# Optimization experiments

Measured on AMD Instinct MI355X. Metric: run time of the kernel, lower is better.

The kernel has to match this reference:

```python
import jax, jax.numpy as jnp
import numpy as np

H = 16
HIDDEN = 1024
B, S = 2, 2048


def setup_inputs() -> dict:
    key = jax.random.key(0)
    ks = jax.random.split(key, 6)
    return {
        "query": jax.random.normal(ks[0], (B, S, HIDDEN), dtype=jnp.float32),
        "key": jax.random.normal(ks[1], (B, S, HIDDEN), dtype=jnp.float32),
        "value": jax.random.normal(ks[2], (B, S, HIDDEN), dtype=jnp.float32),
        "W_query": jax.random.normal(ks[3], (HIDDEN, HIDDEN), dtype=jnp.float32) * 0.01,
        "W_key": jax.random.normal(ks[4], (HIDDEN, HIDDEN), dtype=jnp.float32) * 0.01,
        "W_value": jax.random.normal(ks[5], (HIDDEN, HIDDEN), dtype=jnp.float32) * 0.01,
        "ln_gamma": jnp.ones((HIDDEN,), dtype=jnp.float32),
        "ln_beta": jnp.zeros((HIDDEN,), dtype=jnp.float32),
        "mask": 1,
    }


def reference(query, key, value, W_query, W_key, W_value, ln_gamma, ln_beta, mask):
    b, s, hidden = query.shape
    d = hidden // H  # chunk_size per head
    # project then split last dim into heads, head axis leading: [h, b, s, d]
    def heads(x, W):
        return jnp.transpose((x @ W).reshape(b, s, H, d), (2, 0, 1, 3))
    q = heads(query, W_query)
    k = heads(key, W_key)
    v = heads(value, W_value)
    scale = jnp.asarray(np.sqrt(d), dtype=query.dtype)
    scores = jnp.einsum("hbqd,hbkd->hbqk", q, k) / scale
    aw = jax.nn.softmax(scores, axis=-1)
    if mask:
        tril = jnp.tril(jnp.ones((s, s), dtype=aw.dtype))  # post-softmax mask
        aw = aw * tril
        aw = aw / jnp.sum(aw, axis=3, keepdims=True)
    ws = jnp.einsum("hbqk,hbkd->hbqd", aw, v)
    # concat heads back on last dim: [b, s, hidden]
    ws = jnp.transpose(ws, (1, 2, 0, 3)).reshape(b, s, hidden)
    out = ws + query
    # LayerNorm over last dim, eps=1e-5 (torch default)
    mean = jnp.mean(out, axis=-1, keepdims=True)
    var = jnp.mean(jnp.square(out - mean), axis=-1, keepdims=True)
    out = (out - mean) / jnp.sqrt(var + 1e-5) * ln_gamma + ln_beta
    return out, aw
```

## Files before the change

kernel.cpp:

```cpp
#include <hip/hip_runtime.h>

typedef unsigned short ushort_t;
typedef __attribute__((ext_vector_type(4))) float f32x4;
typedef __attribute__((ext_vector_type(4))) unsigned short u16x4;
typedef __attribute__((ext_vector_type(8))) short short8;
typedef __attribute__((ext_vector_type(8))) unsigned short ushort8;

#define B_DIM 2
#define S_LEN 2048
#define HID 1024
#define NH 16
#define HD 64
#define NROWS (B_DIM * S_LEN)

__device__ __forceinline__ ushort_t f2bf(float f) {
  union { float f; unsigned u; } v; v.f = f;
  unsigned r = v.u + 0x7FFFu + ((v.u >> 16) & 1u);
  return (ushort_t)(r >> 16);
}

__device__ __forceinline__ float bf2f(ushort_t h) {
  union { unsigned u; float f; } v;
  v.u = ((unsigned)h) << 16;
  return v.f;
}

__device__ __forceinline__ f32x4 zero4() {
  f32x4 z = {0.f, 0.f, 0.f, 0.f};
  return z;
}

__device__ __forceinline__ unsigned pk2(float a, float b) {
  unsigned r;
  asm("v_cvt_pk_bf16_f32 %0, %1, %2" : "=v"(r) : "v"(a), "v"(b));
  return r;
}

struct WcArgs { const float* W[3]; ushort_t* T[3]; };

__global__ __launch_bounds__(256) void wconv_kernel(WcArgs args) {
  __shared__ ushort_t L[64 * 65];
  const int k0 = blockIdx.x * 64, n0 = blockIdx.y * 64;
  const float* __restrict__ W = args.W[blockIdx.z];
  ushort_t* __restrict__ T = args.T[blockIdx.z];
  const int tid = threadIdx.x;
  for (int i = 0; i < 4; ++i) {
    int idx = i * 256 + tid;
    int row = idx >> 4;
    int f4  = idx & 15;
    f32x4 v = *(const f32x4*)(W + (size_t)(k0 + row) * HID + n0 + f4 * 4);
    for (int j = 0; j < 4; ++j)
      L[(f4 * 4 + j) * 65 + row] = f2bf(v[j]);
  }
  __syncthreads();
  for (int i = 0; i < 2; ++i) {
    int idx = i * 256 + tid;
    int row = idx >> 3;
    int seg = idx & 7;
    ushort8 u;
    for (int j = 0; j < 8; ++j) u[j] = L[row * 65 + seg * 8 + j];
    *(ushort8*)(T + (size_t)(n0 + row) * HID + k0 + seg * 8) = u;
  }
}

struct PgArgs { const float* A[3]; const ushort_t* Wt[3]; ushort_t* C[3]; };

__global__ __launch_bounds__(256) void proj_gemm(PgArgs args) {
  __shared__ ushort_t As[128 * 64];
  __shared__ ushort_t Bs[128 * 64];
  const int z = blockIdx.z;
  const float* __restrict__ A = args.A[z];
  const ushort_t* __restrict__ Wt = args.Wt[z];
  ushort_t* __restrict__ C = args.C[z];
  const int tid = threadIdx.x;
  const int w = tid >> 6, lane = tid & 63, g = lane >> 4, c = lane & 15;
  const int wm = w >> 1, wn = w & 1;
  const int m0 = blockIdx.y * 128, n0 = blockIdx.x * 128;
  const int swz = (c & 7) << 3;

  f32x4 acc[4][4];
  for (int mi = 0; mi < 4; ++mi)
    for (int ni = 0; ni < 4; ++ni) acc[mi][ni] = zero4();

  for (int kt = 0; kt < 16; ++kt) {
    const int k0 = kt * 64;
    __syncthreads();
    for (int i = 0; i < 4; ++i) {
      int idx = i * 256 + tid;
      int row = idx >> 3, seg = idx & 7;
      const float* src = A + (size_t)(m0 + row) * HID + k0 + seg * 8;
      f32x4 a0 = *(const f32x4*)src;
      f32x4 a1 = *(const f32x4*)(src + 4);
      ushort8 u;
      u[0] = f2bf(a0[0]); u[1] = f2bf(a0[1]); u[2] = f2bf(a0[2]); u[3] = f2bf(a0[3]);
      u[4] = f2bf(a1[0]); u[5] = f2bf(a1[1]); u[6] = f2bf(a1[2]); u[7] = f2bf(a1[3]);
      *(ushort8*)&As[row * 64 + ((seg * 8) ^ ((row & 7) << 3))] = u;
    }
    for (int i = 0; i < 4; ++i) {
      int idx = i * 256 + tid;
      int row = idx >> 3, seg = idx & 7;
      ushort8 u = *(const ushort8*)(Wt + (size_t)(n0 + row) * HID + k0 + seg * 8);
      *(ushort8*)&Bs[row * 64 + ((seg * 8) ^ ((row & 7) << 3))] = u;
    }
    __syncthreads();
    for (int ks = 0; ks < 2; ++ks) {
      short8 af[4], bf4[4];
      for (int mi = 0; mi < 4; ++mi)
        af[mi] = *(const short8*)&As[(wm * 64 + mi * 16 + c) * 64 + ((ks * 32 + 8 * g) ^ swz)];
      for (int ni = 0; ni < 4; ++ni)
        bf4[ni] = *(const short8*)&Bs[(wn * 64 + ni * 16 + c) * 64 + ((ks * 32 + 8 * g) ^ swz)];
      for (int mi = 0; mi < 4; ++mi)
        for (int ni = 0; ni < 4; ++ni)
          acc[mi][ni] = __builtin_amdgcn_mfma_f32_16x16x32_bf16(af[mi], bf4[ni], acc[mi][ni], 0, 0, 0);
    }
  }
  for (int mi = 0; mi < 4; ++mi)
    for (int ni = 0; ni < 4; ++ni)
      for (int r = 0; r < 4; ++r)
        C[(size_t)(m0 + wm * 64 + mi * 16 + 4 * g + r) * HID + n0 + wn * 64 + ni * 16 + c] =
            f2bf(acc[mi][ni][r]);
}

__global__ __launch_bounds__(256) void vtrans_kernel(const ushort_t* __restrict__ Vb,
                                                     ushort_t* __restrict__ VT) {
  __shared__ ushort_t L[64 * 72];
  const int s0 = blockIdx.x * 64, hb = blockIdx.y;
  const int h = hb >> 1, b = hb & 1;
  const int tid = threadIdx.x;
#pragma unroll
  for (int i = 0; i < 2; ++i) {
    int idx = i * 256 + tid;
    int sr = idx >> 3, seg = idx & 7;
    ushort8 u = *(const ushort8*)(Vb + ((size_t)(b * S_LEN) + s0 + sr) * HID + h * HD + seg * 8);
    *(ushort8*)&L[sr * 72 + seg * 8] = u;
  }
  __syncthreads();
#pragma unroll
  for (int i = 0; i < 2; ++i) {
    int idx = i * 256 + tid;
    int d = idx >> 3, seg2 = idx & 7;
    ushort8 u;
#pragma unroll
    for (int j = 0; j < 8; ++j) u[j] = L[(seg2 * 8 + j) * 72 + d];
    *(ushort8*)(VT + ((size_t)hb * HD + d) * S_LEN + s0 + seg2 * 8) = u;
  }
}

#define C2S 0.18033688011112042f

__device__ __forceinline__ void qkt_tile(const ushort_t* Ks, int g, int c,
                                         const short8 qB[2], f32x4 st[4]) {
#pragma unroll
  for (int nf = 0; nf < 4; ++nf) st[nf] = zero4();
#pragma unroll
  for (int ks = 0; ks < 2; ++ks) {
#pragma unroll
    for (int nf = 0; nf < 4; ++nf) {
      short8 kf = *(const short8*)&Ks[(nf * 16 + c) * 64 + 8 * ((4 * ks + g) ^ (c & 7))];
      st[nf] = __builtin_amdgcn_mfma_f32_16x16x32_bf16(kf, qB[ks], st[nf], 0, 0, 0);
    }
  }
}

__device__ __forceinline__ float tile_sum(const f32x4 st[4], int g, int c, int wq, bool diag) {
  float s = 0.f;
#pragma unroll
  for (int nf = 0; nf < 4; ++nf)
#pragma unroll
    for (int r = 0; r < 4; ++r) {
      float e = exp2f(st[nf][r] * C2S);
      bool m = diag && (nf * 16 + 4 * g + r > wq);
      s += m ? 0.f : e;
    }
  return s;
}

__device__ __forceinline__ void tile_p_pv(const f32x4 st[4], float linv, int g, int c,
                                          bool diag, int wq, float* __restrict__ awrow,
                                          char* psb, const short8 vf[2][4], f32x4 oacc[4]) {
#pragma unroll
  for (int nf = 0; nf < 4; ++nf) {
    f32x4 pv;
#pragma unroll
    for (int r = 0; r < 4; ++r) {
      float e = exp2f(st[nf][r] * C2S) * linv;
      bool m = diag && (nf * 16 + 4 * g + r > wq);
      pv[r] = m ? 0.f : e;
    }
    *(f32x4*)(awrow + nf * 16 + 4 * g) = pv;
    uint2 u;
    u.x = pk2(pv[0], pv[1]);
    u.y = pk2(pv[2], pv[3]);
    *(uint2*)(psb + (c * 128 + ((32 * nf + 8 * g) ^ ((c & 7) << 4)))) = u;
  }
#pragma unroll
  for (int ks = 0; ks < 2; ++ks) {
    short8 pf = *(const short8*)(psb + (c * 128 + ((64 * ks + 16 * g) ^ ((c & 7) << 4))));
#pragma unroll
    for (int nf = 0; nf < 4; ++nf)
      oacc[nf] = __builtin_amdgcn_mfma_f32_16x16x32_bf16(vf[ks][nf], pf, oacc[nf], 0, 0, 0);
  }
}

__global__ __launch_bounds__(256) void attn_kernel(const ushort_t* __restrict__ Qb,
    const ushort_t* __restrict__ Kb, const ushort_t* __restrict__ VT,
    float* __restrict__ aw, ushort_t* __restrict__ wsa) {
  __shared__ ushort_t Ks[64 * 64];
  __shared__ ushort_t Vt[64 * 64];
  __shared__ ushort_t Ps[4 * 16 * 64];

  const int tid = threadIdx.x;
  const int w = tid >> 6, lane = tid & 63, g = lane >> 4, c = lane & 15;
  const int p = blockIdx.x, hb = blockIdx.y;
  const int h = hb >> 1, b = hb & 1;
  const int lo = p, hi = 31 - p;
  const int wq = w * 16 + c;
  const int srow = tid >> 3, sseg = tid & 7;

  short8 qlo[2], qhi[2];
  {
    const ushort_t* qp = Qb + ((size_t)(b * S_LEN) + lo * 64 + wq) * HID + h * HD + 8 * g;
    qlo[0] = *(const short8*)qp;
    qlo[1] = *(const short8*)(qp + 32);
    const ushort_t* qp2 = Qb + ((size_t)(b * S_LEN) + hi * 64 + wq) * HID + h * HD + 8 * g;
    qhi[0] = *(const short8*)qp2;
    qhi[1] = *(const short8*)(qp2 + 32);
  }

  ushort8 kr[2], vr[2], kn[2], vn[2];

#pragma unroll
  for (int i = 0; i < 2; ++i) {
    int row = i * 32 + srow;
    kr[i] = *(const ushort8*)(Kb + ((size_t)(b * S_LEN) + row) * HID + h * HD + sseg * 8);
  }
#pragma unroll
  for (int i = 0; i < 2; ++i) {
    int row = i * 32 + srow;
    *(ushort8*)&Ks[row * 64 + 8 * (sseg ^ (row & 7))] = kr[i];
  }
  __syncthreads();

  float ps_lo = 0.f, ps_hi = 0.f;
  for (int kt = 0; kt <= hi; ++kt) {
    if (kt < hi) {
#pragma unroll
      for (int i = 0; i < 2; ++i) {
        int row = i * 32 + srow;
        kn[i] = *(const ushort8*)(Kb + ((size_t)(b * S_LEN) + (kt + 1) * 64 + row) * HID + h * HD + sseg * 8);
      }
    }
    f32x4 st[4];
    qkt_tile(Ks, g, c, qhi, st);
    ps_hi += tile_sum(st, g, c, wq, kt == hi);
    if (kt <= lo) {
      qkt_tile(Ks, g, c, qlo, st);
      ps_lo += tile_sum(st, g, c, wq, kt == lo);
    }
    __syncthreads();
    if (kt < hi) {
#pragma unroll
      for (int i = 0; i < 2; ++i) {
        int row = i * 32 + srow;
        *(ushort8*)&Ks[row * 64 + 8 * (sseg ^ (row & 7))] = kn[i];
      }
    }
    __syncthreads();
  }
  ps_lo += __shfl_xor(ps_lo, 16); ps_lo += __shfl_xor(ps_lo, 32);
  ps_hi += __shfl_xor(ps_hi, 16); ps_hi += __shfl_xor(ps_hi, 32);
  const float linv_lo = 1.0f / ps_lo, linv_hi = 1.0f / ps_hi;

  f32x4 oLo[4], oHi[4];
#pragma unroll
  for (int nf = 0; nf < 4; ++nf) { oLo[nf] = zero4(); oHi[nf] = zero4(); }

#pragma unroll
  for (int i = 0; i < 2; ++i) {
    int row = i * 32 + srow;
    kr[i] = *(const ushort8*)(Kb + ((size_t)(b * S_LEN) + row) * HID + h * HD + sseg * 8);
    vr[i] = *(const ushort8*)(VT + ((size_t)hb * HD + row) * S_LEN + sseg * 8);
  }
#pragma unroll
  for (int i = 0; i < 2; ++i) {
    int row = i * 32 + srow;
    *(ushort8*)&Ks[row * 64 + 8 * (sseg ^ (row & 7))] = kr[i];
    *(ushort8*)&Vt[row * 64 + 8 * (sseg ^ (row & 7))] = vr[i];
  }
  __syncthreads();

  char* psb = (char*)Ps + w * 2048;
  for (int kt = 0; kt <= hi; ++kt) {
    const int kc0 = kt * 64;
    if (kt < hi) {
#pragma unroll
      for (int i = 0; i < 2; ++i) {
        int row = i * 32 + srow;
        kn[i] = *(const ushort8*)(Kb + ((size_t)(b * S_LEN) + kc0 + 64 + row) * HID + h * HD + sseg * 8);
        vn[i] = *(const ushort8*)(VT + ((size_t)hb * HD + row) * S_LEN + kc0 + 64 + sseg * 8);
      }
    }
    short8 vf[2][4];
#pragma unroll
    for (int ks = 0; ks < 2; ++ks)
#pragma unroll
      for (int nf = 0; nf < 4; ++nf)
        vf[ks][nf] = *(const short8*)&Vt[(nf * 16 + c) * 64 + 8 * ((4 * ks + g) ^ (c & 7))];

    f32x4 st[4];
    qkt_tile(Ks, g, c, qhi, st);
    {
      float* awrow = aw + ((size_t)hb * S_LEN + hi * 64 + wq) * S_LEN + kc0;
      tile_p_pv(st, linv_hi, g, c, kt == hi, wq, awrow, psb, vf, oHi);
    }
    if (kt <= lo) {
      qkt_tile(Ks, g, c, qlo, st);
      float* awrow = aw + ((size_t)hb * S_LEN + lo * 64 + wq) * S_LEN + kc0;
      tile_p_pv(st, linv_lo, g, c, kt == lo, wq, awrow, psb, vf, oLo);
    }
    __syncthreads();
    if (kt < hi) {
#pragma unroll
      for (int i = 0; i < 2; ++i) {
        int row = i * 32 + srow;
        *(ushort8*)&Ks[row * 64 + 8 * (sseg ^ (row & 7))] = kn[i];
        *(ushort8*)&Vt[row * 64 + 8 * (sseg ^ (row & 7))] = vn[i];
      }
    }
    __syncthreads();
  }

#pragma unroll
  for (int nf = 0; nf < 4; ++nf) {
    uint2 uh, ul;
    uh.x = pk2(oHi[nf][0], oHi[nf][1]); uh.y = pk2(oHi[nf][2], oHi[nf][3]);
    ul.x = pk2(oLo[nf][0], oLo[nf][1]); ul.y = pk2(oLo[nf][2], oLo[nf][3]);
    *(uint2*)(wsa + ((size_t)(b * S_LEN) + hi * 64 + wq) * HID + h * HD + nf * 16 + 4 * g) = uh;
    *(uint2*)(wsa + ((size_t)(b * S_LEN) + lo * 64 + wq) * HID + h * HD + nf * 16 + 4 * g) = ul;
  }

  const f32x4 zz = zero4();
#pragma unroll
  for (int t = 0; t < 2; ++t) {
    const int tIdx = t ? hi : lo;
    const int z0q = (tIdx + 1) * 16;
    for (int rr = 0; rr < 16; ++rr) {
      f32x4* rowp = (f32x4*)(aw + ((size_t)hb * S_LEN + tIdx * 64 + w * 16 + rr) * S_LEN);
      for (int c4 = z0q + lane; c4 < 512; c4 += 64) rowp[c4] = zz;
    }
  }
}

__global__ __launch_bounds__(256) void ln_kernel(const ushort_t* __restrict__ wsa,
    const float* __restrict__ qin, const float* __restrict__ gamma,
    const float* __restrict__ beta, float* __restrict__ out) {
  __shared__ float red[8];
  const int row = blockIdx.x, tid = threadIdx.x;
  const size_t base = (size_t)row * HID + tid * 4;
  u16x4 xh = *(const u16x4*)(wsa + base);
  f32x4 qv = *(const f32x4*)(qin + base);
  f32x4 x;
  for (int j = 0; j < 4; ++j) x[j] = bf2f(xh[j]) + qv[j];
  float s = x[0] + x[1] + x[2] + x[3];
  float sq = x[0] * x[0] + x[1] * x[1] + x[2] * x[2] + x[3] * x[3];
  for (int m = 1; m <= 32; m <<= 1) {
    s += __shfl_xor(s, m);
    sq += __shfl_xor(sq, m);
  }
  if ((tid & 63) == 0) {
    red[(tid >> 6) * 2] = s;
    red[(tid >> 6) * 2 + 1] = sq;
  }
  __syncthreads();
  s = red[0] + red[2] + red[4] + red[6];
  sq = red[1] + red[3] + red[5] + red[7];
  const float mean = s * (1.0f / HID);
  const float var = sq * (1.0f / HID) - mean * mean;
  const float rstd = 1.0f / sqrtf(var + 1e-5f);
  f32x4 gm = *(const f32x4*)(gamma + tid * 4);
  f32x4 bt = *(const f32x4*)(beta + tid * 4);
  f32x4 o;
  for (int j = 0; j < 4; ++j) o[j] = (x[j] - mean) * rstd * gm[j] + bt[j];
  *(f32x4*)(out + base) = o;
}

extern "C" void kernel_launch(void* const* d_in, const int* in_sizes, int n_in,
                              void* d_out, int out_size, void* d_ws, size_t ws_size,
                              hipStream_t stream) {
  (void)in_sizes; (void)n_in; (void)out_size; (void)ws_size;
  const float* q_in = (const float*)d_in[0];
  const float* k_in = (const float*)d_in[1];
  const float* v_in = (const float*)d_in[2];
  const float* wq   = (const float*)d_in[3];
  const float* wk   = (const float*)d_in[4];
  const float* wv   = (const float*)d_in[5];
  const float* gamma = (const float*)d_in[6];
  const float* beta  = (const float*)d_in[7];

  ushort_t* base = (ushort_t*)d_ws;
  ushort_t* Wt0 = base;
  ushort_t* Wt1 = Wt0 + 1048576;
  ushort_t* Wt2 = Wt1 + 1048576;
  ushort_t* Qb = Wt2 + 1048576;
  ushort_t* Kb = Qb + 4194304;
  ushort_t* Vb = Kb + 4194304;
  ushort_t* VT = Vb + 4194304;
  ushort_t* wsa = VT + 4194304;

  float* out = (float*)d_out;
  float* aw = out + (size_t)NROWS * HID;

  WcArgs wc{{wq, wk, wv}, {Wt0, Wt1, Wt2}};
  wconv_kernel<<<dim3(16, 16, 3), 256, 0, stream>>>(wc);

  PgArgs pg{{q_in, k_in, v_in}, {Wt0, Wt1, Wt2}, {Qb, Kb, Vb}};
  proj_gemm<<<dim3(8, 32, 3), 256, 0, stream>>>(pg);

  vtrans_kernel<<<dim3(32, 32), 256, 0, stream>>>(Vb, VT);

  attn_kernel<<<dim3(16, 32), 256, 0, stream>>>(Qb, Kb, VT, aw, wsa);

  ln_kernel<<<dim3(NROWS), 256, 0, stream>>>(wsa, q_in, gamma, beta, out);
}
```

Baseline: 725.2 us.

## Load K/V fragments directly from global memory, drop LDS staging and barriers

```diff
diff --git a/kernel.cpp b/kernel.cpp
--- a/kernel.cpp
+++ b/kernel.cpp
@@ -148,18 +148,15 @@
 
 #define C2S 0.18033688011112042f
 
-__device__ __forceinline__ void qkt_tile(const ushort_t* Ks, int g, int c,
-                                         const short8 qB[2], f32x4 st[4]) {
+__device__ __forceinline__ void qkt_tile2(const short8 kf[2][4], const short8 qB[2],
+                                          f32x4 st[4]) {
 #pragma unroll
   for (int nf = 0; nf < 4; ++nf) st[nf] = zero4();
 #pragma unroll
-  for (int ks = 0; ks < 2; ++ks) {
-#pragma unroll
-    for (int nf = 0; nf < 4; ++nf) {
-      short8 kf = *(const short8*)&Ks[(nf * 16 + c) * 64 + 8 * ((4 * ks + g) ^ (c & 7))];
-      st[nf] = __builtin_amdgcn_mfma_f32_16x16x32_bf16(kf, qB[ks], st[nf], 0, 0, 0);
-    }
-  }
+  for (int ks = 0; ks < 2; ++ks)
+#pragma unroll
+    for (int nf = 0; nf < 4; ++nf)
+      st[nf] = __builtin_amdgcn_mfma_f32_16x16x32_bf16(kf[ks][nf], qB[ks], st[nf], 0, 0, 0);
 }
 
 __device__ __forceinline__ float tile_sum(const f32x4 st[4], int g, int c, int wq, bool diag) {
@@ -193,6 +190,7 @@
     u.y = pk2(pv[2], pv[3]);
     *(uint2*)(psb + (c * 128 + ((32 * nf + 8 * g) ^ ((c & 7) << 4)))) = u;
   }
+  __builtin_amdgcn_s_setprio(1);
 #pragma unroll
   for (int ks = 0; ks < 2; ++ks) {
     short8 pf = *(const short8*)(psb + (c * 128 + ((64 * ks + 16 * g) ^ ((c & 7) << 4))));
@@ -200,22 +198,22 @@
     for (int nf = 0; nf < 4; ++nf)
       oacc[nf] = __builtin_amdgcn_mfma_f32_16x16x32_bf16(vf[ks][nf], pf, oacc[nf], 0, 0, 0);
   }
+  __builtin_amdgcn_s_setprio(0);
 }
 
 __global__ __launch_bounds__(256) void attn_kernel(const ushort_t* __restrict__ Qb,
     const ushort_t* __restrict__ Kb, const ushort_t* __restrict__ VT,
     float* __restrict__ aw, ushort_t* __restrict__ wsa) {
-  __shared__ ushort_t Ks[64 * 64];
-  __shared__ ushort_t Vt[64 * 64];
   __shared__ ushort_t Ps[4 * 16 * 64];
 
   const int tid = threadIdx.x;
   const int w = tid >> 6, lane = tid & 63, g = lane >> 4, c = lane & 15;
-  const int p = blockIdx.x, hb = blockIdx.y;
+  const int bid = blockIdx.y * 16 + blockIdx.x;
+  const int newid = (bid & 7) * 64 + (bid >> 3);
+  const int p = newid & 15, hb = newid >> 4;
   const int h = hb >> 1, b = hb & 1;
   const int lo = p, hi = 31 - p;
   const int wq = w * 16 + c;
-  const int srow = tid >> 3, sseg = tid & 7;
 
   short8 qlo[2], qhi[2];
   {
@@ -227,45 +225,25 @@
     qhi[1] = *(const short8*)(qp2 + 32);
   }
 
-  ushort8 kr[2], vr[2], kn[2], vn[2];
-
-#pragma unroll
-  for (int i = 0; i < 2; ++i) {
-    int row = i * 32 + srow;
-    kr[i] = *(const ushort8*)(Kb + ((size_t)(b * S_LEN) + row) * HID + h * HD + sseg * 8);
-  }
-#pragma unroll
-  for (int i = 0; i < 2; ++i) {
-    int row = i * 32 + srow;
-    *(ushort8*)&Ks[row * 64 + 8 * (sseg ^ (row & 7))] = kr[i];
-  }
-  __syncthreads();
+  const ushort_t* kbase = Kb + (size_t)(b * S_LEN) * HID + h * HD;
+  const ushort_t* vtb = VT + (size_t)hb * HD * S_LEN;
 
   float ps_lo = 0.f, ps_hi = 0.f;
   for (int kt = 0; kt <= hi; ++kt) {
-    if (kt < hi) {
-#pragma unroll
-      for (int i = 0; i < 2; ++i) {
-        int row = i * 32 + srow;
-        kn[i] = *(const ushort8*)(Kb + ((size_t)(b * S_LEN) + (kt + 1) * 64 + row) * HID + h * HD + sseg * 8);
-      }
-    }
+    short8 kf[2][4];
+#pragma unroll
+    for (int ks = 0; ks < 2; ++ks)
+#pragma unroll
+      for (int nf = 0; nf < 4; ++nf)
+        kf[ks][nf] = *(const short8*)(kbase +
+            (size_t)(kt * 64 + nf * 16 + c) * HID + ks * 32 + 8 * g);
     f32x4 st[4];
-    qkt_tile(Ks, g, c, qhi, st);
+    qkt_tile2(kf, qhi, st);
     ps_hi += tile_sum(st, g, c, wq, kt == hi);
     if (kt <= lo) {
-      qkt_tile(Ks, g, c, qlo, st);
+      qkt_tile2(kf, qlo, st);
       ps_lo += tile_sum(st, g, c, wq, kt == lo);
     }
-    __syncthreads();
-    if (kt < hi) {
-#pragma unroll
-      for (int i = 0; i < 2; ++i) {
-        int row = i * 32 + srow;
-        *(ushort8*)&Ks[row * 64 + 8 * (sseg ^ (row & 7))] = kn[i];
-      }
-    }
-    __syncthreads();
   }
   ps_lo += __shfl_xor(ps_lo, 16); ps_lo += __shfl_xor(ps_lo, 32);
   ps_hi += __shfl_xor(ps_hi, 16); ps_hi += __shfl_xor(ps_hi, 32);
@@ -275,59 +253,30 @@
 #pragma unroll
   for (int nf = 0; nf < 4; ++nf) { oLo[nf] = zero4(); oHi[nf] = zero4(); }
 
-#pragma unroll
-  for (int i = 0; i < 2; ++i) {
-    int row = i * 32 + srow;
-    kr[i] = *(const ushort8*)(Kb + ((size_t)(b * S_LEN) + row) * HID + h * HD + sseg * 8);
-    vr[i] = *(const ushort8*)(VT + ((size_t)hb * HD + row) * S_LEN + sseg * 8);
-  }
-#pragma unroll
-  for (int i = 0; i < 2; ++i) {
-    int row = i * 32 + srow;
-    *(ushort8*)&Ks[row * 64 + 8 * (sseg ^ (row & 7))] = kr[i];
-    *(ushort8*)&Vt[row * 64 + 8 * (sseg ^ (row & 7))] = vr[i];
-  }
-  __syncthreads();
-
   char* psb = (char*)Ps + w * 2048;
   for (int kt = 0; kt <= hi; ++kt) {
     const int kc0 = kt * 64;
-    if (kt < hi) {
-#pragma unroll
-      for (int i = 0; i < 2; ++i) {
-        int row = i * 32 + srow;
-        kn[i] = *(const ushort8*)(Kb + ((size_t)(b * S_LEN) + kc0 + 64 + row) * HID + h * HD + sseg * 8);
-        vn[i] = *(const ushort8*)(VT + ((size_t)hb * HD + row) * S_LEN + kc0 + 64 + sseg * 8);
+    short8 kf[2][4], vf[2][4];
+#pragma unroll
+    for (int ks = 0; ks < 2; ++ks)
+#pragma unroll
+      for (int nf = 0; nf < 4; ++nf) {
+        kf[ks][nf] = *(const short8*)(kbase +
+            (size_t)(kc0 + nf * 16 + c) * HID + ks * 32 + 8 * g);
+        vf[ks][nf] = *(const short8*)(vtb +
+            (size_t)(nf * 16 + c) * S_LEN + kc0 + ks * 32 + 8 * g);
       }
-    }
-    short8 vf[2][4];
-#pragma unroll
-    for (int ks = 0; ks < 2; ++ks)
-#pragma unroll
-      for (int nf = 0; nf < 4; ++nf)
-        vf[ks][nf] = *(const short8*)&Vt[(nf * 16 + c) * 64 + 8 * ((4 * ks + g) ^ (c & 7))];
-
     f32x4 st[4];
-    qkt_tile(Ks, g, c, qhi, st);
+    qkt_tile2(kf, qhi, st);
     {
       float* awrow = aw + ((size_t)hb * S_LEN + hi * 64 + wq) * S_LEN + kc0;
       tile_p_pv(st, linv_hi, g, c, kt == hi, wq, awrow, psb, vf, oHi);
     }
     if (kt <= lo) {
-      qkt_tile(Ks, g, c, qlo, st);
+      qkt_tile2(kf, qlo, st);
       float* awrow = aw + ((size_t)hb * S_LEN + lo * 64 + wq) * S_LEN + kc0;
       tile_p_pv(st, linv_lo, g, c, kt == lo, wq, awrow, psb, vf, oLo);
     }
-    __syncthreads();
-    if (kt < hi) {
-#pragma unroll
-      for (int i = 0; i < 2; ++i) {
-        int row = i * 32 + srow;
-        *(ushort8*)&Ks[row * 64 + 8 * (sseg ^ (row & 7))] = kn[i];
-        *(ushort8*)&Vt[row * 64 + 8 * (sseg ^ (row & 7))] = vn[i];
-      }
-    }
-    __syncthreads();
   }
 
 #pragma unroll
```

Result: slower. 796.1 us (+9.8%).
